# Optimization experiments

Measured on AMD Instinct MI355X. Metric: run time of the kernel, lower is better.

Reference implementation:

```python
import jax, jax.numpy as jnp
import numpy as np

C = 64            # multiplicity of 0e and 1o in in_irreps
N_NODES = 20000
N_EDGES = 320000
RAD_DIM = 8
HID = 64
NUM_IRREPS_OUT = 4 * C   # 2C x 0e + 2C x 1o -> 256 scalar weights
AVG_NUM_NEIGHBORS = 16.0


def setup_inputs() -> dict:
    key = jax.random.key(0)
    ks = jax.random.split(key, 10)
    node_feats = jax.random.normal(ks[0], (N_NODES, C + 3 * C), jnp.float32)
    vectors = jax.random.normal(ks[1], (N_EDGES, 3), jnp.float32)
    radial_embedding = jax.random.normal(ks[2], (N_EDGES, RAD_DIM), jnp.float32)
    senders = jax.random.randint(ks[3], (N_EDGES,), 0, N_NODES, jnp.int32)
    receivers = jax.random.randint(ks[4], (N_EDGES,), 0, N_NODES, jnp.int32)
    # e3nn-style MLP params (no bias), forward scales by 1/sqrt(fan_in)
    W0 = jax.random.normal(ks[5], (RAD_DIM, HID), jnp.float32)
    W1 = jax.random.normal(ks[6], (HID, HID), jnp.float32)
    W2 = jax.random.normal(ks[7], (HID, HID), jnp.float32)
    W3 = jax.random.normal(ks[8], (HID, NUM_IRREPS_OUT), jnp.float32)
    return {"node_feats": node_feats, "vectors": vectors,
            "radial_embedding": radial_embedding, "senders": senders,
            "receivers": receivers, "W0": W0, "W1": W1, "W2": W2, "W3": W3}


def _mlp(x, W0, W1, W2, W3):
    # MultiLayerPerceptron with gradient_normalization=1.0: scale by 1/sqrt(fan_in)
    h = jax.nn.silu(x @ W0 / jnp.sqrt(jnp.asarray(W0.shape[0], x.dtype)))
    h = jax.nn.silu(h @ W1 / jnp.sqrt(jnp.asarray(HID, x.dtype)))
    h = jax.nn.silu(h @ W2 / jnp.sqrt(jnp.asarray(HID, x.dtype)))
    return h @ W3 / jnp.sqrt(jnp.asarray(HID, x.dtype))


def reference(node_feats, vectors, radial_embedding, senders, receivers, W0, W1, W2, W3):
    n = node_feats.shape[0]
    s = node_feats[:, :C]                      # [N, C]  0e block
    v = node_feats[:, C:].reshape(n, C, 3)     # [N, C, 3]  1o block
    s_e = s[senders]                           # gather  [E, C]
    v_e = v[senders]                           # gather  [E, C, 3]
    # spherical harmonics l=1 of -vectors, normalized input, component norm
    r = -vectors
    Y = jnp.sqrt(3.0) * r / jnp.linalg.norm(r, axis=-1, keepdims=True)  # [E, 3]
    # CG tensor product filtered to target irreps (0e + 1o):
    tp_v = s_e[:, :, None] * Y[:, None, :]                 # 0e x 1o -> 1o  [E,C,3]
    tp_s = jnp.einsum('eci,ei->ec', v_e, Y) / jnp.sqrt(3.0)  # 1o x 1o -> 0e  [E,C]
    msg_s = jnp.concatenate([s_e, tp_s], axis=-1)          # [E, 2C]
    msg_v = jnp.concatenate([v_e, tp_v], axis=1)           # [E, 2C, 3]
    # per-irrep MLP gate from radial embedding
    mix = _mlp(radial_embedding, W0, W1, W2, W3)           # [E, 4C]
    msg_s = msg_s * mix[:, :2 * C]
    msg_v = msg_v * mix[:, 2 * C:, None]
    # scatter-add into receivers
    out_s = jnp.zeros((n, 2 * C), msg_s.dtype).at[receivers].add(msg_s)
    out_v = jnp.zeros((n, 2 * C, 3), msg_v.dtype).at[receivers].add(msg_v)
    out = jnp.concatenate([out_s, out_v.reshape(n, 6 * C)], axis=-1)
    return out / AVG_NUM_NEIGHBORS                         # [N, 512]
```

## Files before the change

### kernel.cpp

```cpp
#include <hip/hip_runtime.h>

#define RAD 8
#define HID 64

typedef __attribute__((ext_vector_type(8))) short bf16x8;
typedef __attribute__((ext_vector_type(4))) float f32x4;

static __device__ __forceinline__ unsigned short f2bf(float f) {
    unsigned int u = __float_as_uint(f);
    unsigned int r = (u + 0x7fffu + ((u >> 16) & 1u)) >> 16;
    return (unsigned short)r;
}
static __device__ __forceinline__ float bf2f(unsigned short h) {
    return __uint_as_float(((unsigned int)h) << 16);
}

#define WP_TOTAL 26624

__global__ __launch_bounds__(256) void pack_kernel(
    const float* __restrict__ W0, const float* __restrict__ W1,
    const float* __restrict__ W2, const float* __restrict__ W3,
    unsigned short* __restrict__ Wp)
{
    int o = blockIdx.x * 256 + threadIdx.x;
    if (o >= WP_TOTAL) return;
    float val;
    if (o < 2048) {
        int nt = o >> 9, w = o & 511, lane = w >> 3, j = w & 7;
        int k = (lane >> 4) * 8 + j, n = nt * 16 + (lane & 15);
        val = (k < 8) ? W0[k * 64 + n] * 0.35355339059327373f : 0.f;
    } else if (o < 6144) {
        int oo = o - 2048, fid = oo >> 9, w = oo & 511, lane = w >> 3, j = w & 7;
        int nt = fid >> 1, ks = fid & 1;
        int k = ks * 32 + (lane >> 4) * 8 + j, n = nt * 16 + (lane & 15);
        val = W1[k * 64 + n] * 0.125f;
    } else if (o < 10240) {
        int oo = o - 6144, fid = oo >> 9, w = oo & 511, lane = w >> 3, j = w & 7;
        int nt = fid >> 1, ks = fid & 1;
        int k = ks * 32 + (lane >> 4) * 8 + j, n = nt * 16 + (lane & 15);
        val = W2[k * 64 + n] * 0.125f;
    } else {
        int oo = o - 10240, fid = oo >> 9, w = oo & 511, lane = w >> 3, j = w & 7;
        int nt = fid >> 1, ks = fid & 1;
        int k = ks * 32 + (lane >> 4) * 8 + j, n = nt * 16 + (lane & 15);
        val = W3[k * 256 + n] * 0.125f;
    }
    Wp[o] = f2bf(val);
}

__global__ __launch_bounds__(256) void mlp_mfma_kernel(
    const float* __restrict__ radial,
    const unsigned short* __restrict__ Wp,
    unsigned short* __restrict__ mix,
    int E)
{
    __shared__ unsigned short sWp[WP_TOTAL];
    __shared__ unsigned short sH[4][1024];

    const int t = threadIdx.x;
    {
        int4* dst = (int4*)sWp;
        const int4* src = (const int4*)Wp;
        #pragma unroll
        for (int i = 0; i < 13; ++i) dst[t + i * 256] = src[t + i * 256];
    }
    __syncthreads();

    const int wv = t >> 6, l = t & 63;
    const int lrow = l & 15;
    const int quad = l >> 4;
    const int e0 = blockIdx.x * 64 + wv * 16;
    if (e0 >= E) return;
    int nval = E - e0; if (nval > 16) nval = 16;

    unsigned short* H = sH[wv];

    bf16x8 a0 = {0, 0, 0, 0, 0, 0, 0, 0};
    if (quad == 0 && lrow < nval) {
        const float* rr = radial + (size_t)(e0 + lrow) * 8;
        #pragma unroll
        for (int j = 0; j < 8; ++j) a0[j] = (short)f2bf(rr[j]);
    }
    {
        f32x4 c[4];
        #pragma unroll
        for (int nt = 0; nt < 4; ++nt) {
            bf16x8 b = *(const bf16x8*)(sWp + nt * 512 + l * 8);
            f32x4 z = {0.f, 0.f, 0.f, 0.f};
            c[nt] = __builtin_amdgcn_mfma_f32_16x16x32_bf16(a0, b, z, 0, 0, 0);
        }
        #pragma unroll
        for (int nt = 0; nt < 4; ++nt) {
            #pragma unroll
            for (int r = 0; r < 4; ++r) {
                float v = c[nt][r];
                float h = v / (1.f + __expf(-v));
                int er = quad * 4 + r;
                int f  = nt * 16 + lrow;
                H[er * 64 + (f ^ ((er & 7) << 3))] = f2bf(h);
            }
        }
    }

    #pragma unroll 1
    for (int L = 0; L < 2; ++L) {
        const unsigned short* WL = sWp + 2048 + L * 4096;
        bf16x8 a[2];
        #pragma unroll
        for (int ks = 0; ks < 2; ++ks)
            a[ks] = *(const bf16x8*)(H + lrow * 64 + ((ks * 32 + quad * 8) ^ ((lrow & 7) << 3)));
        f32x4 c[4];
        #pragma unroll
        for (int nt = 0; nt < 4; ++nt) { f32x4 z = {0.f,0.f,0.f,0.f}; c[nt] = z; }
        #pragma unroll
        for (int ks = 0; ks < 2; ++ks) {
            #pragma unroll
            for (int nt = 0; nt < 4; ++nt) {
                bf16x8 b = *(const bf16x8*)(WL + (nt * 2 + ks) * 512 + l * 8);
                c[nt] = __builtin_amdgcn_mfma_f32_16x16x32_bf16(a[ks], b, c[nt], 0, 0, 0);
            }
        }
        #pragma unroll
        for (int nt = 0; nt < 4; ++nt) {
            #pragma unroll
            for (int r = 0; r < 4; ++r) {
                float v = c[nt][r];
                float h = v / (1.f + __expf(-v));
                int er = quad * 4 + r;
                int f  = nt * 16 + lrow;
                H[er * 64 + (f ^ ((er & 7) << 3))] = f2bf(h);
            }
        }
    }

    {
        const unsigned short* WL = sWp + 10240;
        bf16x8 a[2];
        #pragma unroll
        for (int ks = 0; ks < 2; ++ks)
            a[ks] = *(const bf16x8*)(H + lrow * 64 + ((ks * 32 + quad * 8) ^ ((lrow & 7) << 3)));
        #pragma unroll 1
        for (int g = 0; g < 4; ++g) {
            f32x4 c[4];
            #pragma unroll
            for (int np = 0; np < 4; ++np) { f32x4 z = {0.f,0.f,0.f,0.f}; c[np] = z; }
            #pragma unroll
            for (int ks = 0; ks < 2; ++ks) {
                #pragma unroll
                for (int np = 0; np < 4; ++np) {
                    int nt = g * 4 + np;
                    bf16x8 b = *(const bf16x8*)(WL + (nt * 2 + ks) * 512 + l * 8);
                    c[np] = __builtin_amdgcn_mfma_f32_16x16x32_bf16(a[ks], b, c[np], 0, 0, 0);
                }
            }
            #pragma unroll
            for (int np = 0; np < 4; ++np) {
                #pragma unroll
                for (int r = 0; r < 4; ++r) {
                    int er = quad * 4 + r;
                    if (er < nval) {
                        int f = (g * 4 + np) * 16 + lrow;
                        mix[(size_t)(e0 + er) * 256 + f] = f2bf(c[np][r]);
                    }
                }
            }
        }
    }
}

__global__ __launch_bounds__(256) void hist_kernel(const int* __restrict__ recv,
                                                   int* __restrict__ cnt, int E)
{
    int i = blockIdx.x * 256 + threadIdx.x;
    if (i < E) atomicAdd(&cnt[recv[i]], 1);
}

__global__ __launch_bounds__(1024) void scan_kernel(const int* __restrict__ cnt,
                                                    int* __restrict__ off,
                                                    int* __restrict__ cursor, int N)
{
    __shared__ int part[1024];
    int t = threadIdx.x;
    int per = (N + 1023) / 1024;
    int base = t * per;
    int s = 0;
    for (int i = 0; i < per; ++i) { int idx = base + i; if (idx < N) s += cnt[idx]; }
    part[t] = s;
    __syncthreads();
    for (int d = 1; d < 1024; d <<= 1) {
        int v = (t >= d) ? part[t - d] : 0;
        __syncthreads();
        part[t] += v;
        __syncthreads();
    }
    int run = (t == 0) ? 0 : part[t - 1];
    for (int i = 0; i < per; ++i) {
        int idx = base + i;
        if (idx < N) { off[idx] = run; cursor[idx] = run; run += cnt[idx]; }
    }
    if (t == 1023) off[N] = part[1023];
}

__global__ __launch_bounds__(256) void fill_kernel(const int* __restrict__ recv,
                                                   int* __restrict__ cursor,
                                                   int* __restrict__ edge_of, int E)
{
    int i = blockIdx.x * 256 + threadIdx.x;
    if (i < E) {
        int p = atomicAdd(&cursor[recv[i]], 1);
        edge_of[p] = i;
    }
}

__global__ __launch_bounds__(256) void gather_kernel(
    const float* __restrict__ node_feats,
    const float* __restrict__ vectors,
    const int*   __restrict__ senders,
    const int*   __restrict__ edge_of,
    const int*   __restrict__ off,
    const unsigned short* __restrict__ mix,
    float* __restrict__ out, int N)
{
    int wid  = threadIdx.x >> 6;
    int lane = threadIdx.x & 63;
    int n = blockIdx.x * 4 + wid;
    if (n >= N) return;

    int beg = off[n], end = off[n + 1];

    float a0 = 0.f, a1 = 0.f;
    float b0 = 0.f, b1 = 0.f, b2 = 0.f;
    float c0 = 0.f, c1 = 0.f, c2 = 0.f;

    const float s3  = 1.7320508075688772f;
    const float is3 = 0.5773502691896258f;

    #pragma unroll 2
    for (int i = beg; i < end; ++i) {
        int e   = edge_of[i];
        int snd = senders[e];

        float r0 = -vectors[(size_t)e * 3 + 0];
        float r1 = -vectors[(size_t)e * 3 + 1];
        float r2 = -vectors[(size_t)e * 3 + 2];
        float inv = rsqrtf(r0 * r0 + r1 * r1 + r2 * r2);
        float Y0 = s3 * r0 * inv, Y1 = s3 * r1 * inv, Y2 = s3 * r2 * inv;

        const float* nf = node_feats + (size_t)snd * 256;
        float s_e = nf[lane];
        float v0  = nf[64 + lane * 3 + 0];
        float v1  = nf[64 + lane * 3 + 1];
        float v2  = nf[64 + lane * 3 + 2];

        const unsigned short* m = mix + (size_t)e * 256;
        float m0 = bf2f(m[lane]);
        float m1 = bf2f(m[64 + lane]);
        float m2 = bf2f(m[128 + lane]);
        float m3 = bf2f(m[192 + lane]);

        float tp_s = (v0 * Y0 + v1 * Y1 + v2 * Y2) * is3;

        a0 += s_e * m0;
        a1 += tp_s * m1;
        b0 += v0 * m2; b1 += v1 * m2; b2 += v2 * m2;
        float sm = s_e * m3;
        c0 += Y0 * sm; c1 += Y1 * sm; c2 += Y2 * sm;
    }

    float* o = out + (size_t)n * 512;
    const float kk = 0.0625f;
    o[lane]      = a0 * kk;
    o[64 + lane] = a1 * kk;
    o[128 + lane * 3 + 0] = b0 * kk;
    o[128 + lane * 3 + 1] = b1 * kk;
    o[128 + lane * 3 + 2] = b2 * kk;
    o[320 + lane * 3 + 0] = c0 * kk;
    o[320 + lane * 3 + 1] = c1 * kk;
    o[320 + lane * 3 + 2] = c2 * kk;
}

__global__ __launch_bounds__(256) void mlp_kernel(
    const float* __restrict__ radial,
    const float* __restrict__ W0g, const float* __restrict__ W1g,
    const float* __restrict__ W2g, const float* __restrict__ W3g,
    unsigned short* __restrict__ mix, int e1)
{
    __shared__ float  sHf[HID * 256];
    __shared__ float4 sW4[1024];

    const int t = threadIdx.x;
    const int e = blockIdx.x * 256 + t;
    const bool valid = e < e1;

    if (t < 128) sW4[t] = ((const float4*)W0g)[t];
    __syncthreads();

    float x[8];
    if (valid) {
        float4 ra = ((const float4*)radial)[(size_t)e * 2 + 0];
        float4 rb = ((const float4*)radial)[(size_t)e * 2 + 1];
        x[0]=ra.x; x[1]=ra.y; x[2]=ra.z; x[3]=ra.w;
        x[4]=rb.x; x[5]=rb.y; x[6]=rb.z; x[7]=rb.w;
    } else {
        #pragma unroll
        for (int k = 0; k < 8; ++k) x[k] = 0.f;
    }

    float acc[64];
    #pragma unroll
    for (int j = 0; j < 64; ++j) acc[j] = 0.f;
    #pragma unroll
    for (int k = 0; k < 8; ++k) {
        #pragma unroll
        for (int jq = 0; jq < 16; ++jq) {
            float4 w = sW4[k * 16 + jq];
            acc[jq*4+0] = fmaf(x[k], w.x, acc[jq*4+0]);
            acc[jq*4+1] = fmaf(x[k], w.y, acc[jq*4+1]);
            acc[jq*4+2] = fmaf(x[k], w.z, acc[jq*4+2]);
            acc[jq*4+3] = fmaf(x[k], w.w, acc[jq*4+3]);
        }
    }
    #pragma unroll
    for (int j = 0; j < 64; ++j) {
        float v = acc[j] * 0.35355339059327373f;
        sHf[j * 256 + t] = v / (1.f + __expf(-v));
    }
    __syncthreads();
    #pragma unroll
    for (int i = 0; i < 4; ++i) sW4[t + i * 256] = ((const float4*)W1g)[t + i * 256];
    __syncthreads();

    #pragma unroll
    for (int j = 0; j < 64; ++j) acc[j] = 0.f;
    #pragma unroll 2
    for (int k = 0; k < 64; ++k) {
        float hk = sHf[k * 256 + t];
        #pragma unroll
        for (int jq = 0; jq < 16; ++jq) {
            float4 w = sW4[k * 16 + jq];
            acc[jq*4+0] = fmaf(hk, w.x, acc[jq*4+0]);
            acc[jq*4+1] = fmaf(hk, w.y, acc[jq*4+1]);
            acc[jq*4+2] = fmaf(hk, w.z, acc[jq*4+2]);
            acc[jq*4+3] = fmaf(hk, w.w, acc[jq*4+3]);
        }
    }
    __syncthreads();
    #pragma unroll
    for (int i = 0; i < 4; ++i) sW4[t + i * 256] = ((const float4*)W2g)[t + i * 256];
    #pragma unroll
    for (int j = 0; j < 64; ++j) {
        float v = acc[j] * 0.125f;
        sHf[j * 256 + t] = v / (1.f + __expf(-v));
    }
    __syncthreads();

    #pragma unroll
    for (int j = 0; j < 64; ++j) acc[j] = 0.f;
    #pragma unroll 2
    for (int k = 0; k < 64; ++k) {
        float hk = sHf[k * 256 + t];
        #pragma unroll
        for (int jq = 0; jq < 16; ++jq) {
            float4 w = sW4[k * 16 + jq];
            acc[jq*4+0] = fmaf(hk, w.x, acc[jq*4+0]);
            acc[jq*4+1] = fmaf(hk, w.y, acc[jq*4+1]);
            acc[jq*4+2] = fmaf(hk, w.z, acc[jq*4+2]);
            acc[jq*4+3] = fmaf(hk, w.w, acc[jq*4+3]);
        }
    }
    __syncthreads();
    #pragma unroll
    for (int j = 0; j < 64; ++j) {
        float v = acc[j] * 0.125f;
        sHf[j * 256 + t] = v / (1.f + __expf(-v));
    }

    unsigned short* mrow = mix + (size_t)e * 256;
    #pragma unroll 1
    for (int jt = 0; jt < 4; ++jt) {
        #pragma unroll
        for (int i = 0; i < 4; ++i) {
            int m = t + i * 256;
            sW4[m] = ((const float4*)W3g)[(m >> 4) * 64 + jt * 16 + (m & 15)];
        }
        __syncthreads();

        #pragma unroll
        for (int j = 0; j < 64; ++j) acc[j] = 0.f;
        #pragma unroll 2
        for (int k = 0; k < 64; ++k) {
            float hk = sHf[k * 256 + t];
            #pragma unroll
            for (int jq = 0; jq < 16; ++jq) {
                float4 w = sW4[k * 16 + jq];
                acc[jq*4+0] = fmaf(hk, w.x, acc[jq*4+0]);
                acc[jq*4+1] = fmaf(hk, w.y, acc[jq*4+1]);
                acc[jq*4+2] = fmaf(hk, w.z, acc[jq*4+2]);
                acc[jq*4+3] = fmaf(hk, w.w, acc[jq*4+3]);
            }
        }
        if (valid) {
            #pragma unroll
            for (int j4 = 0; j4 < 16; ++j4) {
                ushort4 u;
                u.x = f2bf(acc[j4*4+0] * 0.125f);
                u.y = f2bf(acc[j4*4+1] * 0.125f);
                u.z = f2bf(acc[j4*4+2] * 0.125f);
                u.w = f2bf(acc[j4*4+3] * 0.125f);
                *reinterpret_cast<ushort4*>(&mrow[jt * 64 + j4 * 4]) = u;
            }
        }
        __syncthreads();
    }
}

__global__ __launch_bounds__(256) void scatter_kernel(
    const float* __restrict__ node_feats,
    const float* __restrict__ vectors,
    const int*   __restrict__ senders,
    const int*   __restrict__ receivers,
    const unsigned short* __restrict__ mix,
    float* __restrict__ out, int e0, int e1)
{
    int wid  = threadIdx.x >> 6;
    int lane = threadIdx.x & 63;
    int e = e0 + blockIdx.x * 4 + wid;
    if (e >= e1) return;

    int snd = senders[e];
    int rcv = receivers[e];

    float r0 = -vectors[(size_t)e * 3 + 0];
    float r1 = -vectors[(size_t)e * 3 + 1];
    float r2 = -vectors[(size_t)e * 3 + 2];
    float inv = rsqrtf(r0 * r0 + r1 * r1 + r2 * r2);
    float Y0 = 1.7320508075688772f * r0 * inv;
    float Y1 = 1.7320508075688772f * r1 * inv;
    float Y2 = 1.7320508075688772f * r2 * inv;

    const float* nf = node_feats + (size_t)snd * 256;
    float s_e = nf[lane];
    float v0 = nf[64 + lane * 3 + 0];
    float v1 = nf[64 + lane * 3 + 1];
    float v2 = nf[64 + lane * 3 + 2];

    float tp_s = (v0 * Y0 + v1 * Y1 + v2 * Y2) * 0.5773502691896258f;

    const unsigned short* m = mix + (size_t)(e - e0) * 256;
    float m0 = bf2f(m[lane]), m1 = bf2f(m[64 + lane]);
    float m2 = bf2f(m[128 + lane]), m3 = bf2f(m[192 + lane]);

    float* orow = out + (size_t)rcv * 512;
    const float kk = 0.0625f;
    atomicAdd(&orow[lane],      s_e  * m0 * kk);
    atomicAdd(&orow[64 + lane], tp_s * m1 * kk);
    float mv = m2 * kk;
    atomicAdd(&orow[128 + lane * 3 + 0], v0 * mv);
    atomicAdd(&orow[128 + lane * 3 + 1], v1 * mv);
    atomicAdd(&orow[128 + lane * 3 + 2], v2 * mv);
    float ms = s_e * m3 * kk;
    atomicAdd(&orow[320 + lane * 3 + 0], Y0 * ms);
    atomicAdd(&orow[320 + lane * 3 + 1], Y1 * ms);
    atomicAdd(&orow[320 + lane * 3 + 2], Y2 * ms);
}

extern "C" void kernel_launch(void* const* d_in, const int* in_sizes, int n_in,
                              void* d_out, int out_size, void* d_ws, size_t ws_size,
                              hipStream_t stream)
{
    const float* node_feats = (const float*)d_in[0];
    const float* vectors    = (const float*)d_in[1];
    const float* radial     = (const float*)d_in[2];
    const int*   senders    = (const int*)d_in[3];
    const int*   receivers  = (const int*)d_in[4];
    const float* W0         = (const float*)d_in[5];
    const float* W1         = (const float*)d_in[6];
    const float* W2         = (const float*)d_in[7];
    const float* W3         = (const float*)d_in[8];
    float* out = (float*)d_out;

    const int E = in_sizes[3];
    const int N = in_sizes[0] / 256;

    size_t mix_bytes = (size_t)E * 256 * sizeof(unsigned short);
    size_t mix_al    = (mix_bytes + 255) & ~(size_t)255;
    size_t int_bytes = (size_t)(N + (N + 1) + N + E) * sizeof(int);
    size_t int_al    = (int_bytes + 255) & ~(size_t)255;
    size_t wp_bytes  = (size_t)WP_TOTAL * sizeof(unsigned short);
    size_t need      = mix_al + int_al + wp_bytes;

    if (ws_size >= need) {
        unsigned short* mix = (unsigned short*)d_ws;
        int* cnt      = (int*)((char*)d_ws + mix_al);
        int* off      = cnt + N;
        int* cursor   = off + (N + 1);
        int* edge_of  = cursor + N;
        unsigned short* Wp = (unsigned short*)((char*)d_ws + mix_al + int_al);

        hipMemsetAsync(cnt, 0, (size_t)N * sizeof(int), stream);

        pack_kernel<<<dim3((WP_TOTAL + 255) / 256), dim3(256), 0, stream>>>(
            W0, W1, W2, W3, Wp);
        mlp_mfma_kernel<<<dim3((E + 63) / 64), dim3(256), 0, stream>>>(
            radial, Wp, mix, E);

        hist_kernel<<<dim3((E + 255) / 256), dim3(256), 0, stream>>>(receivers, cnt, E);
        scan_kernel<<<dim3(1), dim3(1024), 0, stream>>>(cnt, off, cursor, N);
        fill_kernel<<<dim3((E + 255) / 256), dim3(256), 0, stream>>>(receivers, cursor, edge_of, E);

        gather_kernel<<<dim3((N + 3) / 4), dim3(256), 0, stream>>>(
            node_feats, vectors, senders, edge_of, off, mix, out, N);
    } else {
        hipMemsetAsync(d_out, 0, (size_t)out_size * sizeof(float), stream);
        size_t per_edge = 256 * sizeof(unsigned short);
        long long chunk_ll = (long long)(ws_size / per_edge);
        int chunk = (chunk_ll > E) ? E : (int)chunk_ll;
        chunk &= ~255;
        if (chunk <= 0) chunk = 256;
        unsigned short* mix = (unsigned short*)d_ws;
        for (int s = 0; s < E; s += chunk) {
            int eend = s + chunk; if (eend > E) eend = E;
            int ne = eend - s;
            mlp_kernel<<<dim3((ne + 255) / 256), dim3(256), 0, stream>>>(
                radial + (size_t)s * 8, W0, W1, W2, W3, mix, ne);
            scatter_kernel<<<dim3((ne + 3) / 4), dim3(256), 0, stream>>>(
                node_feats, vectors, senders, receivers, mix, out, s, eend);
        }
    }
}
```

Before: 232.5 us.

## Fuse radial MLP into per-node gather kernel and merge weight packing with histogram

Removes the separate MLP kernel and its E×256 bf16 mix buffer. Each wave now computes the MLP gates on the fly for chunks of 16 incoming edges of its node using MFMA, stages them in shared memory, and accumulates the messages directly. Weight packing and the receiver histogram are merged into one launch. This cuts global traffic for the mix tensor and one or two launches, at the cost of padded MFMA work for low-degree chunks, re-reading edge data twice per chunk, and fused-kernel W3 fragments being read from global rather than shared memory.

```diff
diff --git a/kernel.cpp b/kernel.cpp
--- a/kernel.cpp
+++ b/kernel.cpp
@@ -1,7 +1,4 @@
 #include <hip/hip_runtime.h>
-
-#define RAD 8
-#define HID 64
 
 typedef __attribute__((ext_vector_type(8))) short bf16x8;
 typedef __attribute__((ext_vector_type(4))) float f32x4;
@@ -17,162 +14,38 @@
 
 #define WP_TOTAL 26624
 
-__global__ __launch_bounds__(256) void pack_kernel(
+__global__ __launch_bounds__(256) void prep_kernel(
     const float* __restrict__ W0, const float* __restrict__ W1,
     const float* __restrict__ W2, const float* __restrict__ W3,
-    unsigned short* __restrict__ Wp)
+    unsigned short* __restrict__ Wp,
+    const int* __restrict__ recv, int* __restrict__ cnt, int E)
 {
     int o = blockIdx.x * 256 + threadIdx.x;
-    if (o >= WP_TOTAL) return;
-    float val;
-    if (o < 2048) {
-        int nt = o >> 9, w = o & 511, lane = w >> 3, j = w & 7;
-        int k = (lane >> 4) * 8 + j, n = nt * 16 + (lane & 15);
-        val = (k < 8) ? W0[k * 64 + n] * 0.35355339059327373f : 0.f;
-    } else if (o < 6144) {
-        int oo = o - 2048, fid = oo >> 9, w = oo & 511, lane = w >> 3, j = w & 7;
-        int nt = fid >> 1, ks = fid & 1;
-        int k = ks * 32 + (lane >> 4) * 8 + j, n = nt * 16 + (lane & 15);
-        val = W1[k * 64 + n] * 0.125f;
-    } else if (o < 10240) {
-        int oo = o - 6144, fid = oo >> 9, w = oo & 511, lane = w >> 3, j = w & 7;
-        int nt = fid >> 1, ks = fid & 1;
-        int k = ks * 32 + (lane >> 4) * 8 + j, n = nt * 16 + (lane & 15);
-        val = W2[k * 64 + n] * 0.125f;
-    } else {
-        int oo = o - 10240, fid = oo >> 9, w = oo & 511, lane = w >> 3, j = w & 7;
-        int nt = fid >> 1, ks = fid & 1;
-        int k = ks * 32 + (lane >> 4) * 8 + j, n = nt * 16 + (lane & 15);
-        val = W3[k * 256 + n] * 0.125f;
-    }
-    Wp[o] = f2bf(val);
-}
-
-__global__ __launch_bounds__(256) void mlp_mfma_kernel(
-    const float* __restrict__ radial,
-    const unsigned short* __restrict__ Wp,
-    unsigned short* __restrict__ mix,
-    int E)
-{
-    __shared__ unsigned short sWp[WP_TOTAL];
-    __shared__ unsigned short sH[4][1024];
-
-    const int t = threadIdx.x;
-    {
-        int4* dst = (int4*)sWp;
-        const int4* src = (const int4*)Wp;
-        #pragma unroll
-        for (int i = 0; i < 13; ++i) dst[t + i * 256] = src[t + i * 256];
-    }
-    __syncthreads();
-
-    const int wv = t >> 6, l = t & 63;
-    const int lrow = l & 15;
-    const int quad = l >> 4;
-    const int e0 = blockIdx.x * 64 + wv * 16;
-    if (e0 >= E) return;
-    int nval = E - e0; if (nval > 16) nval = 16;
-
-    unsigned short* H = sH[wv];
-
-    bf16x8 a0 = {0, 0, 0, 0, 0, 0, 0, 0};
-    if (quad == 0 && lrow < nval) {
-        const float* rr = radial + (size_t)(e0 + lrow) * 8;
-        #pragma unroll
-        for (int j = 0; j < 8; ++j) a0[j] = (short)f2bf(rr[j]);
-    }
-    {
-        f32x4 c[4];
-        #pragma unroll
-        for (int nt = 0; nt < 4; ++nt) {
-            bf16x8 b = *(const bf16x8*)(sWp + nt * 512 + l * 8);
-            f32x4 z = {0.f, 0.f, 0.f, 0.f};
-            c[nt] = __builtin_amdgcn_mfma_f32_16x16x32_bf16(a0, b, z, 0, 0, 0);
-        }
-        #pragma unroll
-        for (int nt = 0; nt < 4; ++nt) {
-            #pragma unroll
-            for (int r = 0; r < 4; ++r) {
-                float v = c[nt][r];
-                float h = v / (1.f + __expf(-v));
-                int er = quad * 4 + r;
-                int f  = nt * 16 + lrow;
-                H[er * 64 + (f ^ ((er & 7) << 3))] = f2bf(h);
-            }
-        }
-    }
-
-    #pragma unroll 1
-    for (int L = 0; L < 2; ++L) {
-        const unsigned short* WL = sWp + 2048 + L * 4096;
-        bf16x8 a[2];
-        #pragma unroll
-        for (int ks = 0; ks < 2; ++ks)
-            a[ks] = *(const bf16x8*)(H + lrow * 64 + ((ks * 32 + quad * 8) ^ ((lrow & 7) << 3)));
-        f32x4 c[4];
-        #pragma unroll
-        for (int nt = 0; nt < 4; ++nt) { f32x4 z = {0.f,0.f,0.f,0.f}; c[nt] = z; }
-        #pragma unroll
-        for (int ks = 0; ks < 2; ++ks) {
-            #pragma unroll
-            for (int nt = 0; nt < 4; ++nt) {
-                bf16x8 b = *(const bf16x8*)(WL + (nt * 2 + ks) * 512 + l * 8);
-                c[nt] = __builtin_amdgcn_mfma_f32_16x16x32_bf16(a[ks], b, c[nt], 0, 0, 0);
-            }
-        }
-        #pragma unroll
-        for (int nt = 0; nt < 4; ++nt) {
-            #pragma unroll
-            for (int r = 0; r < 4; ++r) {
-                float v = c[nt][r];
-                float h = v / (1.f + __expf(-v));
-                int er = quad * 4 + r;
-                int f  = nt * 16 + lrow;
-                H[er * 64 + (f ^ ((er & 7) << 3))] = f2bf(h);
-            }
-        }
-    }
-
-    {
-        const unsigned short* WL = sWp + 10240;
-        bf16x8 a[2];
-        #pragma unroll
-        for (int ks = 0; ks < 2; ++ks)
-            a[ks] = *(const bf16x8*)(H + lrow * 64 + ((ks * 32 + quad * 8) ^ ((lrow & 7) << 3)));
-        #pragma unroll 1
-        for (int g = 0; g < 4; ++g) {
-            f32x4 c[4];
-            #pragma unroll
-            for (int np = 0; np < 4; ++np) { f32x4 z = {0.f,0.f,0.f,0.f}; c[np] = z; }
-            #pragma unroll
-            for (int ks = 0; ks < 2; ++ks) {
-                #pragma unroll
-                for (int np = 0; np < 4; ++np) {
-                    int nt = g * 4 + np;
-                    bf16x8 b = *(const bf16x8*)(WL + (nt * 2 + ks) * 512 + l * 8);
-                    c[np] = __builtin_amdgcn_mfma_f32_16x16x32_bf16(a[ks], b, c[np], 0, 0, 0);
-                }
-            }
-            #pragma unroll
-            for (int np = 0; np < 4; ++np) {
-                #pragma unroll
-                for (int r = 0; r < 4; ++r) {
-                    int er = quad * 4 + r;
-                    if (er < nval) {
-                        int f = (g * 4 + np) * 16 + lrow;
-                        mix[(size_t)(e0 + er) * 256 + f] = f2bf(c[np][r]);
-                    }
-                }
-            }
-        }
-    }
-}
-
-__global__ __launch_bounds__(256) void hist_kernel(const int* __restrict__ recv,
-                                                   int* __restrict__ cnt, int E)
-{
-    int i = blockIdx.x * 256 + threadIdx.x;
-    if (i < E) atomicAdd(&cnt[recv[i]], 1);
+    if (o < WP_TOTAL) {
+        float val;
+        if (o < 2048) {
+            int nt = o >> 9, w = o & 511, lane = w >> 3, j = w & 7;
+            int k = (lane >> 4) * 8 + j, n = nt * 16 + (lane & 15);
+            val = (k < 8) ? W0[k * 64 + n] * 0.35355339059327373f : 0.f;
+        } else if (o < 6144) {
+            int oo = o - 2048, fid = oo >> 9, w = oo & 511, lane = w >> 3, j = w & 7;
+            int nt = fid >> 1, ks = fid & 1;
+            int k = ks * 32 + (lane >> 4) * 8 + j, n = nt * 16 + (lane & 15);
+            val = W1[k * 64 + n] * 0.125f;
+        } else if (o < 10240) {
+            int oo = o - 6144, fid = oo >> 9, w = oo & 511, lane = w >> 3, j = w & 7;
+            int nt = fid >> 1, ks = fid & 1;
+            int k = ks * 32 + (lane >> 4) * 8 + j, n = nt * 16 + (lane & 15);
+            val = W2[k * 64 + n] * 0.125f;
+        } else {
+            int oo = o - 10240, fid = oo >> 9, w = oo & 511, lane = w >> 3, j = w & 7;
+            int nt = fid >> 1, ks = fid & 1;
+            int k = ks * 32 + (lane >> 4) * 8 + j, n = nt * 16 + (lane & 15);
+            val = W3[k * 256 + n] * 0.125f;
+        }
+        Wp[o] = f2bf(val);
+    }
+    if (o < E) atomicAdd(&cnt[recv[o]], 1);
 }
 
 __global__ __launch_bounds__(1024) void scan_kernel(const int* __restrict__ cnt,
@@ -212,73 +85,205 @@
     }
 }
 
-__global__ __launch_bounds__(256) void gather_kernel(
+__global__ __launch_bounds__(256) void fused_kernel(
     const float* __restrict__ node_feats,
     const float* __restrict__ vectors,
+    const float* __restrict__ radial,
     const int*   __restrict__ senders,
     const int*   __restrict__ edge_of,
     const int*   __restrict__ off,
-    const unsigned short* __restrict__ mix,
+    const unsigned short* __restrict__ Wp,
     float* __restrict__ out, int N)
 {
-    int wid  = threadIdx.x >> 6;
-    int lane = threadIdx.x & 63;
-    int n = blockIdx.x * 4 + wid;
+    __shared__ __align__(16) unsigned short sW[10240];
+    __shared__ __align__(16) unsigned short sH[4][1024];
+    __shared__ __align__(16) unsigned short sM[4][2048];
+
+    const int t = threadIdx.x;
+    {
+        int4* dst = (int4*)sW;
+        const int4* src = (const int4*)Wp;
+        #pragma unroll
+        for (int i = 0; i < 5; ++i) dst[t + i * 256] = src[t + i * 256];
+    }
+    __syncthreads();
+
+    const int wv = t >> 6, l = t & 63;
+    const int lrow = l & 15, quad = l >> 4;
+    const int n = blockIdx.x * 4 + wv;
     if (n >= N) return;
 
-    int beg = off[n], end = off[n + 1];
-
-    float a0 = 0.f, a1 = 0.f;
+    const int beg = off[n];
+    const int deg = off[n + 1] - beg;
+
+    unsigned short* H = sH[wv];
+    unsigned short* M = sM[wv];
+
+    float a0s = 0.f, a1s = 0.f;
     float b0 = 0.f, b1 = 0.f, b2 = 0.f;
     float c0 = 0.f, c1 = 0.f, c2 = 0.f;
-
     const float s3  = 1.7320508075688772f;
     const float is3 = 0.5773502691896258f;
 
-    #pragma unroll 2
-    for (int i = beg; i < end; ++i) {
-        int e   = edge_of[i];
-        int snd = senders[e];
-
-        float r0 = -vectors[(size_t)e * 3 + 0];
-        float r1 = -vectors[(size_t)e * 3 + 1];
-        float r2 = -vectors[(size_t)e * 3 + 2];
-        float inv = rsqrtf(r0 * r0 + r1 * r1 + r2 * r2);
-        float Y0 = s3 * r0 * inv, Y1 = s3 * r1 * inv, Y2 = s3 * r2 * inv;
-
-        const float* nf = node_feats + (size_t)snd * 256;
-        float s_e = nf[lane];
-        float v0  = nf[64 + lane * 3 + 0];
-        float v1  = nf[64 + lane * 3 + 1];
-        float v2  = nf[64 + lane * 3 + 2];
-
-        const unsigned short* m = mix + (size_t)e * 256;
-        float m0 = bf2f(m[lane]);
-        float m1 = bf2f(m[64 + lane]);
-        float m2 = bf2f(m[128 + lane]);
-        float m3 = bf2f(m[192 + lane]);
-
-        float tp_s = (v0 * Y0 + v1 * Y1 + v2 * Y2) * is3;
-
-        a0 += s_e * m0;
-        a1 += tp_s * m1;
-        b0 += v0 * m2; b1 += v1 * m2; b2 += v2 * m2;
-        float sm = s_e * m3;
-        c0 += Y0 * sm; c1 += Y1 * sm; c2 += Y2 * sm;
+    const unsigned short* W3 = Wp + 10240;
+
+    for (int c16 = 0; c16 < deg; c16 += 16) {
+        int cdeg = deg - c16; if (cdeg > 16) cdeg = 16;
+
+        bf16x8 afr = {0, 0, 0, 0, 0, 0, 0, 0};
+        if (quad == 0) {
+            int i = c16 + lrow; if (i >= deg) i = deg - 1;
+            int e = edge_of[beg + i];
+            const float* rr = radial + (size_t)e * 8;
+            float4 ra = *(const float4*)rr;
+            float4 rb = *(const float4*)(rr + 4);
+            afr[0] = (short)f2bf(ra.x); afr[1] = (short)f2bf(ra.y);
+            afr[2] = (short)f2bf(ra.z); afr[3] = (short)f2bf(ra.w);
+            afr[4] = (short)f2bf(rb.x); afr[5] = (short)f2bf(rb.y);
+            afr[6] = (short)f2bf(rb.z); afr[7] = (short)f2bf(rb.w);
+        }
+        #pragma unroll
+        for (int nt = 0; nt < 4; ++nt) {
+            bf16x8 b = *(const bf16x8*)(sW + nt * 512 + l * 8);
+            f32x4 z = {0.f, 0.f, 0.f, 0.f};
+            f32x4 cf = __builtin_amdgcn_mfma_f32_16x16x32_bf16(afr, b, z, 0, 0, 0);
+            #pragma unroll
+            for (int r = 0; r < 4; ++r) {
+                float v = cf[r];
+                float h = v / (1.f + __expf(-v));
+                int er = quad * 4 + r;
+                int f  = nt * 16 + lrow;
+                H[er * 64 + (f ^ ((er & 7) << 3))] = f2bf(h);
+            }
+        }
+
+        #pragma unroll 1
+        for (int L = 0; L < 2; ++L) {
+            const unsigned short* WL = sW + 2048 + L * 4096;
+            bf16x8 a[2];
+            #pragma unroll
+            for (int ks = 0; ks < 2; ++ks)
+                a[ks] = *(const bf16x8*)(H + lrow * 64 + ((ks * 32 + quad * 8) ^ ((lrow & 7) << 3)));
+            f32x4 cf[4];
+            #pragma unroll
+            for (int nt = 0; nt < 4; ++nt) { f32x4 z = {0.f,0.f,0.f,0.f}; cf[nt] = z; }
+            #pragma unroll
+            for (int ks = 0; ks < 2; ++ks) {
+                #pragma unroll
+                for (int nt = 0; nt < 4; ++nt) {
+                    bf16x8 b = *(const bf16x8*)(WL + (nt * 2 + ks) * 512 + l * 8);
+                    cf[nt] = __builtin_amdgcn_mfma_f32_16x16x32_bf16(a[ks], b, cf[nt], 0, 0, 0);
+                }
+            }
+            #pragma unroll
+            for (int nt = 0; nt < 4; ++nt) {
+                #pragma unroll
+                for (int r = 0; r < 4; ++r) {
+                    float v = cf[nt][r];
+                    float h = v / (1.f + __expf(-v));
+                    int er = quad * 4 + r;
+                    int f  = nt * 16 + lrow;
+                    H[er * 64 + (f ^ ((er & 7) << 3))] = f2bf(h);
+                }
+            }
+        }
+
+        bf16x8 a3[2];
+        #pragma unroll
+        for (int ks = 0; ks < 2; ++ks)
+            a3[ks] = *(const bf16x8*)(H + lrow * 64 + ((ks * 32 + quad * 8) ^ ((lrow & 7) << 3)));
+
+        auto do_g = [&](int g, int slot) {
+            f32x4 cf[4];
+            #pragma unroll
+            for (int np = 0; np < 4; ++np) { f32x4 z = {0.f,0.f,0.f,0.f}; cf[np] = z; }
+            #pragma unroll
+            for (int ks = 0; ks < 2; ++ks) {
+                #pragma unroll
+                for (int np = 0; np < 4; ++np) {
+                    int nt = g * 4 + np;
+                    bf16x8 b = *(const bf16x8*)(W3 + (nt * 2 + ks) * 512 + l * 8);
+                    cf[np] = __builtin_amdgcn_mfma_f32_16x16x32_bf16(a3[ks], b, cf[np], 0, 0, 0);
+                }
+            }
+            #pragma unroll
+            for (int np = 0; np < 4; ++np) {
+                int c2 = np * 16 + lrow;
+                ushort4 u;
+                u.x = f2bf(cf[np][0]); u.y = f2bf(cf[np][1]);
+                u.z = f2bf(cf[np][2]); u.w = f2bf(cf[np][3]);
+                *(ushort4*)&M[slot * 1024 + c2 * 16 + ((quad * 4) ^ (c2 & 12))] = u;
+            }
+        };
+
+        do_g(1, 0);
+        do_g(2, 1);
+        #pragma unroll
+        for (int er4 = 0; er4 < 4; ++er4) {
+            ushort4 m1v = *(const ushort4*)&M[0 * 1024 + l * 16 + ((er4 * 4) ^ (l & 12))];
+            ushort4 m2v = *(const ushort4*)&M[1 * 1024 + l * 16 + ((er4 * 4) ^ (l & 12))];
+            float f1[4] = { bf2f(m1v.x), bf2f(m1v.y), bf2f(m1v.z), bf2f(m1v.w) };
+            float f2[4] = { bf2f(m2v.x), bf2f(m2v.y), bf2f(m2v.z), bf2f(m2v.w) };
+            #pragma unroll
+            for (int r = 0; r < 4; ++r) {
+                int er = er4 * 4 + r;
+                if (er < cdeg) {
+                    int e   = edge_of[beg + c16 + er];
+                    int snd = senders[e];
+                    float r0 = -vectors[(size_t)e * 3 + 0];
+                    float r1 = -vectors[(size_t)e * 3 + 1];
+                    float r2 = -vectors[(size_t)e * 3 + 2];
+                    float inv = rsqrtf(r0 * r0 + r1 * r1 + r2 * r2);
+                    float Y0 = s3 * r0 * inv, Y1 = s3 * r1 * inv, Y2 = s3 * r2 * inv;
+                    const float* nf = node_feats + (size_t)snd * 256 + 64 + l * 3;
+                    float v0 = nf[0], v1 = nf[1], v2 = nf[2];
+                    a1s += (v0 * Y0 + v1 * Y1 + v2 * Y2) * is3 * f1[r];
+                    b0 += v0 * f2[r]; b1 += v1 * f2[r]; b2 += v2 * f2[r];
+                }
+            }
+        }
+
+        do_g(0, 0);
+        do_g(3, 1);
+        #pragma unroll
+        for (int er4 = 0; er4 < 4; ++er4) {
+            ushort4 m0v = *(const ushort4*)&M[0 * 1024 + l * 16 + ((er4 * 4) ^ (l & 12))];
+            ushort4 m3v = *(const ushort4*)&M[1 * 1024 + l * 16 + ((er4 * 4) ^ (l & 12))];
+            float f0[4] = { bf2f(m0v.x), bf2f(m0v.y), bf2f(m0v.z), bf2f(m0v.w) };
+            float f3[4] = { bf2f(m3v.x), bf2f(m3v.y), bf2f(m3v.z), bf2f(m3v.w) };
+            #pragma unroll
+            for (int r = 0; r < 4; ++r) {
+                int er = er4 * 4 + r;
+                if (er < cdeg) {
+                    int e   = edge_of[beg + c16 + er];
+                    int snd = senders[e];
+                    float r0 = -vectors[(size_t)e * 3 + 0];
+                    float r1 = -vectors[(size_t)e * 3 + 1];
+                    float r2 = -vectors[(size_t)e * 3 + 2];
+                    float inv = rsqrtf(r0 * r0 + r1 * r1 + r2 * r2);
+                    float Y0 = s3 * r0 * inv, Y1 = s3 * r1 * inv, Y2 = s3 * r2 * inv;
+                    float s_e = node_feats[(size_t)snd * 256 + l];
+                    a0s += s_e * f0[r];
+                    float sm = s_e * f3[r];
+                    c0 += Y0 * sm; c1 += Y1 * sm; c2 += Y2 * sm;
+                }
+            }
+        }
     }
 
     float* o = out + (size_t)n * 512;
     const float kk = 0.0625f;
-    o[lane]      = a0 * kk;
-    o[64 + lane] = a1 * kk;
-    o[128 + lane * 3 + 0] = b0 * kk;
-    o[128 + lane * 3 + 1] = b1 * kk;
-    o[128 + lane * 3 + 2] = b2 * kk;
-    o[320 + lane * 3 + 0] = c0 * kk;
-    o[320 + lane * 3 + 1] = c1 * kk;
-    o[320 + lane * 3 + 2] = c2 * kk;
-}
-
+    o[l]      = a0s * kk;
+    o[64 + l] = a1s * kk;
+    o[128 + l * 3 + 0] = b0 * kk;
+    o[128 + l * 3 + 1] = b1 * kk;
+    o[128 + l * 3 + 2] = b2 * kk;
+    o[320 + l * 3 + 0] = c0 * kk;
+    o[320 + l * 3 + 1] = c1 * kk;
+    o[320 + l * 3 + 2] = c2 * kk;
+}
+
+#define HID 64
 __global__ __launch_bounds__(256) void mlp_kernel(
     const float* __restrict__ radial,
     const float* __restrict__ W0g, const float* __restrict__ W1g,
@@ -482,34 +487,27 @@
     const int E = in_sizes[3];
     const int N = in_sizes[0] / 256;
 
-    size_t mix_bytes = (size_t)E * 256 * sizeof(unsigned short);
-    size_t mix_al    = (mix_bytes + 255) & ~(size_t)255;
     size_t int_bytes = (size_t)(N + (N + 1) + N + E) * sizeof(int);
     size_t int_al    = (int_bytes + 255) & ~(size_t)255;
     size_t wp_bytes  = (size_t)WP_TOTAL * sizeof(unsigned short);
-    size_t need      = mix_al + int_al + wp_bytes;
+    size_t need      = int_al + wp_bytes;
 
     if (ws_size >= need) {
-        unsigned short* mix = (unsigned short*)d_ws;
-        int* cnt      = (int*)((char*)d_ws + mix_al);
+        int* cnt      = (int*)d_ws;
         int* off      = cnt + N;
         int* cursor   = off + (N + 1);
         int* edge_of  = cursor + N;
-        unsigned short* Wp = (unsigned short*)((char*)d_ws + mix_al + int_al);
+        unsigned short* Wp = (unsigned short*)((char*)d_ws + int_al);
 
         hipMemsetAsync(cnt, 0, (size_t)N * sizeof(int), stream);
 
-        pack_kernel<<<dim3((WP_TOTAL + 255) / 256), dim3(256), 0, stream>>>(
-            W0, W1, W2, W3, Wp);
-        mlp_mfma_kernel<<<dim3((E + 63) / 64), dim3(256), 0, stream>>>(
-            radial, Wp, mix, E);
-
-        hist_kernel<<<dim3((E + 255) / 256), dim3(256), 0, stream>>>(receivers, cnt, E);
+        prep_kernel<<<dim3((E + 255) / 256), dim3(256), 0, stream>>>(
+            W0, W1, W2, W3, Wp, receivers, cnt, E);
         scan_kernel<<<dim3(1), dim3(1024), 0, stream>>>(cnt, off, cursor, N);
         fill_kernel<<<dim3((E + 255) / 256), dim3(256), 0, stream>>>(receivers, cursor, edge_of, E);
 
-        gather_kernel<<<dim3((N + 3) / 4), dim3(256), 0, stream>>>(
-            node_feats, vectors, senders, edge_of, off, mix, out, N);
+        fused_kernel<<<dim3((N + 3) / 4), dim3(256), 0, stream>>>(
+            node_feats, vectors, radial, senders, edge_of, off, Wp, out, N);
     } else {
         hipMemsetAsync(d_out, 0, (size_t)out_size * sizeof(float), stream);
         size_t per_edge = 256 * sizeof(unsigned short);
```

New measurement: 489.2 us. +110.4%, slower.

## Compute MLP mix in receiver-sorted order and fuse weight pack with histogram

Applied to the files above, without the earlier changes.

The MLP kernel now runs after the CSR build and writes mix rows in receiver-sorted position order, reading radial rows through edge_of. The gather kernel then reads mix contiguously by position rather than by random edge id. Weight packing and the receiver histogram are merged into one launch. W3 is read from global memory instead of shared memory to cut LDS use, and output rows are staged through LDS for wider 8-byte stores. The cost is a gather of radial inputs and the MLP losing the chance to overlap with the sort kernels.

```diff
diff --git a/kernel.cpp b/kernel.cpp
--- a/kernel.cpp
+++ b/kernel.cpp
@@ -1,7 +1,4 @@
 #include <hip/hip_runtime.h>
-
-#define RAD 8
-#define HID 64
 
 typedef __attribute__((ext_vector_type(8))) short bf16x8;
 typedef __attribute__((ext_vector_type(4))) float f32x4;
@@ -17,162 +14,38 @@
 
 #define WP_TOTAL 26624
 
-__global__ __launch_bounds__(256) void pack_kernel(
+__global__ __launch_bounds__(256) void prep_kernel(
     const float* __restrict__ W0, const float* __restrict__ W1,
     const float* __restrict__ W2, const float* __restrict__ W3,
-    unsigned short* __restrict__ Wp)
+    unsigned short* __restrict__ Wp,
+    const int* __restrict__ recv, int* __restrict__ cnt, int E)
 {
     int o = blockIdx.x * 256 + threadIdx.x;
-    if (o >= WP_TOTAL) return;
-    float val;
-    if (o < 2048) {
-        int nt = o >> 9, w = o & 511, lane = w >> 3, j = w & 7;
-        int k = (lane >> 4) * 8 + j, n = nt * 16 + (lane & 15);
-        val = (k < 8) ? W0[k * 64 + n] * 0.35355339059327373f : 0.f;
-    } else if (o < 6144) {
-        int oo = o - 2048, fid = oo >> 9, w = oo & 511, lane = w >> 3, j = w & 7;
-        int nt = fid >> 1, ks = fid & 1;
-        int k = ks * 32 + (lane >> 4) * 8 + j, n = nt * 16 + (lane & 15);
-        val = W1[k * 64 + n] * 0.125f;
-    } else if (o < 10240) {
-        int oo = o - 6144, fid = oo >> 9, w = oo & 511, lane = w >> 3, j = w & 7;
-        int nt = fid >> 1, ks = fid & 1;
-        int k = ks * 32 + (lane >> 4) * 8 + j, n = nt * 16 + (lane & 15);
-        val = W2[k * 64 + n] * 0.125f;
-    } else {
-        int oo = o - 10240, fid = oo >> 9, w = oo & 511, lane = w >> 3, j = w & 7;
-        int nt = fid >> 1, ks = fid & 1;
-        int k = ks * 32 + (lane >> 4) * 8 + j, n = nt * 16 + (lane & 15);
-        val = W3[k * 256 + n] * 0.125f;
-    }
-    Wp[o] = f2bf(val);
-}
-
-__global__ __launch_bounds__(256) void mlp_mfma_kernel(
-    const float* __restrict__ radial,
-    const unsigned short* __restrict__ Wp,
-    unsigned short* __restrict__ mix,
-    int E)
-{
-    __shared__ unsigned short sWp[WP_TOTAL];
-    __shared__ unsigned short sH[4][1024];
-
-    const int t = threadIdx.x;
-    {
-        int4* dst = (int4*)sWp;
-        const int4* src = (const int4*)Wp;
-        #pragma unroll
-        for (int i = 0; i < 13; ++i) dst[t + i * 256] = src[t + i * 256];
-    }
-    __syncthreads();
-
-    const int wv = t >> 6, l = t & 63;
-    const int lrow = l & 15;
-    const int quad = l >> 4;
-    const int e0 = blockIdx.x * 64 + wv * 16;
-    if (e0 >= E) return;
-    int nval = E - e0; if (nval > 16) nval = 16;
-
-    unsigned short* H = sH[wv];
-
-    bf16x8 a0 = {0, 0, 0, 0, 0, 0, 0, 0};
-    if (quad == 0 && lrow < nval) {
-        const float* rr = radial + (size_t)(e0 + lrow) * 8;
-        #pragma unroll
-        for (int j = 0; j < 8; ++j) a0[j] = (short)f2bf(rr[j]);
-    }
-    {
-        f32x4 c[4];
-        #pragma unroll
-        for (int nt = 0; nt < 4; ++nt) {
-            bf16x8 b = *(const bf16x8*)(sWp + nt * 512 + l * 8);
-            f32x4 z = {0.f, 0.f, 0.f, 0.f};
-            c[nt] = __builtin_amdgcn_mfma_f32_16x16x32_bf16(a0, b, z, 0, 0, 0);
-        }
-        #pragma unroll
-        for (int nt = 0; nt < 4; ++nt) {
-            #pragma unroll
-            for (int r = 0; r < 4; ++r) {
-                float v = c[nt][r];
-                float h = v / (1.f + __expf(-v));
-                int er = quad * 4 + r;
-                int f  = nt * 16 + lrow;
-                H[er * 64 + (f ^ ((er & 7) << 3))] = f2bf(h);
-            }
-        }
-    }
-
-    #pragma unroll 1
-    for (int L = 0; L < 2; ++L) {
-        const unsigned short* WL = sWp + 2048 + L * 4096;
-        bf16x8 a[2];
-        #pragma unroll
-        for (int ks = 0; ks < 2; ++ks)
-            a[ks] = *(const bf16x8*)(H + lrow * 64 + ((ks * 32 + quad * 8) ^ ((lrow & 7) << 3)));
-        f32x4 c[4];
-        #pragma unroll
-        for (int nt = 0; nt < 4; ++nt) { f32x4 z = {0.f,0.f,0.f,0.f}; c[nt] = z; }
-        #pragma unroll
-        for (int ks = 0; ks < 2; ++ks) {
-            #pragma unroll
-            for (int nt = 0; nt < 4; ++nt) {
-                bf16x8 b = *(const bf16x8*)(WL + (nt * 2 + ks) * 512 + l * 8);
-                c[nt] = __builtin_amdgcn_mfma_f32_16x16x32_bf16(a[ks], b, c[nt], 0, 0, 0);
-            }
-        }
-        #pragma unroll
-        for (int nt = 0; nt < 4; ++nt) {
-            #pragma unroll
-            for (int r = 0; r < 4; ++r) {
-                float v = c[nt][r];
-                float h = v / (1.f + __expf(-v));
-                int er = quad * 4 + r;
-                int f  = nt * 16 + lrow;
-                H[er * 64 + (f ^ ((er & 7) << 3))] = f2bf(h);
-            }
-        }
-    }
-
-    {
-        const unsigned short* WL = sWp + 10240;
-        bf16x8 a[2];
-        #pragma unroll
-        for (int ks = 0; ks < 2; ++ks)
-            a[ks] = *(const bf16x8*)(H + lrow * 64 + ((ks * 32 + quad * 8) ^ ((lrow & 7) << 3)));
-        #pragma unroll 1
-        for (int g = 0; g < 4; ++g) {
-            f32x4 c[4];
-            #pragma unroll
-            for (int np = 0; np < 4; ++np) { f32x4 z = {0.f,0.f,0.f,0.f}; c[np] = z; }
-            #pragma unroll
-            for (int ks = 0; ks < 2; ++ks) {
-                #pragma unroll
-                for (int np = 0; np < 4; ++np) {
-                    int nt = g * 4 + np;
-                    bf16x8 b = *(const bf16x8*)(WL + (nt * 2 + ks) * 512 + l * 8);
-                    c[np] = __builtin_amdgcn_mfma_f32_16x16x32_bf16(a[ks], b, c[np], 0, 0, 0);
-                }
-            }
-            #pragma unroll
-            for (int np = 0; np < 4; ++np) {
-                #pragma unroll
-                for (int r = 0; r < 4; ++r) {
-                    int er = quad * 4 + r;
-                    if (er < nval) {
-                        int f = (g * 4 + np) * 16 + lrow;
-                        mix[(size_t)(e0 + er) * 256 + f] = f2bf(c[np][r]);
-                    }
-                }
-            }
-        }
-    }
-}
-
-__global__ __launch_bounds__(256) void hist_kernel(const int* __restrict__ recv,
-                                                   int* __restrict__ cnt, int E)
-{
-    int i = blockIdx.x * 256 + threadIdx.x;
-    if (i < E) atomicAdd(&cnt[recv[i]], 1);
+    if (o < WP_TOTAL) {
+        float val;
+        if (o < 2048) {
+            int nt = o >> 9, w = o & 511, lane = w >> 3, j = w & 7;
+            int k = (lane >> 4) * 8 + j, n = nt * 16 + (lane & 15);
+            val = (k < 8) ? W0[k * 64 + n] * 0.35355339059327373f : 0.f;
+        } else if (o < 6144) {
+            int oo = o - 2048, fid = oo >> 9, w = oo & 511, lane = w >> 3, j = w & 7;
+            int nt = fid >> 1, ks = fid & 1;
+            int k = ks * 32 + (lane >> 4) * 8 + j, n = nt * 16 + (lane & 15);
+            val = W1[k * 64 + n] * 0.125f;
+        } else if (o < 10240) {
+            int oo = o - 6144, fid = oo >> 9, w = oo & 511, lane = w >> 3, j = w & 7;
+            int nt = fid >> 1, ks = fid & 1;
+            int k = ks * 32 + (lane >> 4) * 8 + j, n = nt * 16 + (lane & 15);
+            val = W2[k * 64 + n] * 0.125f;
+        } else {
+            int oo = o - 10240, fid = oo >> 9, w = oo & 511, lane = w >> 3, j = w & 7;
+            int nt = fid >> 1, ks = fid & 1;
+            int k = ks * 32 + (lane >> 4) * 8 + j, n = nt * 16 + (lane & 15);
+            val = W3[k * 256 + n] * 0.125f;
+        }
+        Wp[o] = f2bf(val);
+    }
+    if (o < E) atomicAdd(&cnt[recv[o]], 1);
 }
 
 __global__ __launch_bounds__(1024) void scan_kernel(const int* __restrict__ cnt,
@@ -209,6 +82,129 @@
     if (i < E) {
         int p = atomicAdd(&cursor[recv[i]], 1);
         edge_of[p] = i;
+    }
+}
+
+__global__ __launch_bounds__(256) void mlp_pos_kernel(
+    const float* __restrict__ radial,
+    const int* __restrict__ edge_of,
+    const unsigned short* __restrict__ Wp,
+    unsigned short* __restrict__ mix,
+    int E)
+{
+    __shared__ __align__(16) unsigned short sW[10240];
+    __shared__ __align__(16) unsigned short sH[4][1024];
+    __shared__ __align__(16) unsigned short sM[4][16 * 68];
+
+    const int t = threadIdx.x;
+    {
+        int4* dst = (int4*)sW;
+        const int4* src = (const int4*)Wp;
+        #pragma unroll
+        for (int i = 0; i < 5; ++i) dst[t + i * 256] = src[t + i * 256];
+    }
+    __syncthreads();
+
+    const int wv = t >> 6, l = t & 63;
+    const int lrow = l & 15, quad = l >> 4;
+    const int p0 = blockIdx.x * 64 + wv * 16;
+    if (p0 >= E) return;
+
+    unsigned short* H = sH[wv];
+    unsigned short* M = sM[wv];
+
+    bf16x8 afr = {0, 0, 0, 0, 0, 0, 0, 0};
+    if (quad == 0) {
+        int i = p0 + lrow; if (i >= E) i = E - 1;
+        int e = edge_of[i];
+        const float* rr = radial + (size_t)e * 8;
+        float4 ra = *(const float4*)rr;
+        float4 rb = *(const float4*)(rr + 4);
+        afr[0] = (short)f2bf(ra.x); afr[1] = (short)f2bf(ra.y);
+        afr[2] = (short)f2bf(ra.z); afr[3] = (short)f2bf(ra.w);
+        afr[4] = (short)f2bf(rb.x); afr[5] = (short)f2bf(rb.y);
+        afr[6] = (short)f2bf(rb.z); afr[7] = (short)f2bf(rb.w);
+    }
+    #pragma unroll
+    for (int nt = 0; nt < 4; ++nt) {
+        bf16x8 b = *(const bf16x8*)(sW + nt * 512 + l * 8);
+        f32x4 z = {0.f, 0.f, 0.f, 0.f};
+        f32x4 cf = __builtin_amdgcn_mfma_f32_16x16x32_bf16(afr, b, z, 0, 0, 0);
+        #pragma unroll
+        for (int r = 0; r < 4; ++r) {
+            float v = cf[r];
+            float h = v / (1.f + __expf(-v));
+            int er = quad * 4 + r;
+            int f  = nt * 16 + lrow;
+            H[er * 64 + (f ^ ((er & 7) << 3))] = f2bf(h);
+        }
+    }
+
+    #pragma unroll 1
+    for (int L = 0; L < 2; ++L) {
+        const unsigned short* WL = sW + 2048 + L * 4096;
+        bf16x8 a[2];
+        #pragma unroll
+        for (int ks = 0; ks < 2; ++ks)
+            a[ks] = *(const bf16x8*)(H + lrow * 64 + ((ks * 32 + quad * 8) ^ ((lrow & 7) << 3)));
+        f32x4 cf[4];
+        #pragma unroll
+        for (int nt = 0; nt < 4; ++nt) { f32x4 z = {0.f,0.f,0.f,0.f}; cf[nt] = z; }
+        #pragma unroll
+        for (int ks = 0; ks < 2; ++ks) {
+            #pragma unroll
+            for (int nt = 0; nt < 4; ++nt) {
+                bf16x8 b = *(const bf16x8*)(WL + (nt * 2 + ks) * 512 + l * 8);
+                cf[nt] = __builtin_amdgcn_mfma_f32_16x16x32_bf16(a[ks], b, cf[nt], 0, 0, 0);
+            }
+        }
+        #pragma unroll
+        for (int nt = 0; nt < 4; ++nt) {
+            #pragma unroll
+            for (int r = 0; r < 4; ++r) {
+                float v = cf[nt][r];
+                float h = v / (1.f + __expf(-v));
+                int er = quad * 4 + r;
+                int f  = nt * 16 + lrow;
+                H[er * 64 + (f ^ ((er & 7) << 3))] = f2bf(h);
+            }
+        }
+    }
+
+    bf16x8 a3[2];
+    #pragma unroll
+    for (int ks = 0; ks < 2; ++ks)
+        a3[ks] = *(const bf16x8*)(H + lrow * 64 + ((ks * 32 + quad * 8) ^ ((lrow & 7) << 3)));
+
+    const unsigned short* W3 = Wp + 10240;
+    #pragma unroll 1
+    for (int g = 0; g < 4; ++g) {
+        f32x4 cf[4];
+        #pragma unroll
+        for (int np = 0; np < 4; ++np) { f32x4 z = {0.f,0.f,0.f,0.f}; cf[np] = z; }
+        #pragma unroll
+        for (int ks = 0; ks < 2; ++ks) {
+            #pragma unroll
+            for (int np = 0; np < 4; ++np) {
+                int nt = g * 4 + np;
+                bf16x8 b = *(const bf16x8*)(W3 + (nt * 2 + ks) * 512 + l * 8);
+                cf[np] = __builtin_amdgcn_mfma_f32_16x16x32_bf16(a3[ks], b, cf[np], 0, 0, 0);
+            }
+        }
+        #pragma unroll
+        for (int np = 0; np < 4; ++np) {
+            int c2 = np * 16 + lrow;
+            #pragma unroll
+            for (int r = 0; r < 4; ++r)
+                M[(quad * 4 + r) * 68 + c2] = f2bf(cf[np][r]);
+        }
+        #pragma unroll
+        for (int i = 0; i < 4; ++i) {
+            int ri = i * 4 + quad;
+            ushort4 v = *(const ushort4*)&M[ri * 68 + lrow * 4];
+            if (p0 + ri < E)
+                *(ushort4*)&mix[(size_t)(p0 + ri) * 256 + g * 64 + lrow * 4] = v;
+        }
     }
 }
 
@@ -252,7 +248,7 @@
         float v1  = nf[64 + lane * 3 + 1];
         float v2  = nf[64 + lane * 3 + 2];
 
-        const unsigned short* m = mix + (size_t)e * 256;
+        const unsigned short* m = mix + (size_t)i * 256;
         float m0 = bf2f(m[lane]);
         float m1 = bf2f(m[64 + lane]);
         float m2 = bf2f(m[128 + lane]);
@@ -279,6 +275,7 @@
     o[320 + lane * 3 + 2] = c2 * kk;
 }
 
+#define HID 64
 __global__ __launch_bounds__(256) void mlp_kernel(
     const float* __restrict__ radial,
     const float* __restrict__ W0g, const float* __restrict__ W1g,
@@ -499,14 +496,13 @@
 
         hipMemsetAsync(cnt, 0, (size_t)N * sizeof(int), stream);
 
-        pack_kernel<<<dim3((WP_TOTAL + 255) / 256), dim3(256), 0, stream>>>(
-            W0, W1, W2, W3, Wp);
-        mlp_mfma_kernel<<<dim3((E + 63) / 64), dim3(256), 0, stream>>>(
-            radial, Wp, mix, E);
-
-        hist_kernel<<<dim3((E + 255) / 256), dim3(256), 0, stream>>>(receivers, cnt, E);
+        prep_kernel<<<dim3((E + 255) / 256), dim3(256), 0, stream>>>(
+            W0, W1, W2, W3, Wp, receivers, cnt, E);
         scan_kernel<<<dim3(1), dim3(1024), 0, stream>>>(cnt, off, cursor, N);
         fill_kernel<<<dim3((E + 255) / 256), dim3(256), 0, stream>>>(receivers, cursor, edge_of, E);
+
+        mlp_pos_kernel<<<dim3((E + 63) / 64), dim3(256), 0, stream>>>(
+            radial, edge_of, Wp, mix, E);
 
         gather_kernel<<<dim3((N + 3) / 4), dim3(256), 0, stream>>>(
             node_feats, vectors, senders, edge_of, off, mix, out, N);
```

Result: faster. 221.2 us (-4.8%).
